# Optimization experiments

Measured on AMD Instinct MI355X. Metric: run time of the kernel, lower is better.

Reference implementation:

```python
import jax, jax.numpy as jnp
import numpy as np

B, L, H, E, R, T = 256, 100, 1000, 100, 247, 15


def setup_inputs() -> dict:
    key = jax.random.key(0)
    ks = jax.random.split(key, 16)
    g = lambda i, shape, s=0.05: jax.random.normal(ks[i], shape, dtype=jnp.float32) * s
    z = lambda *shape: jnp.zeros(shape, jnp.float32)
    return {
        "emb_seq": g(0, (B, T, E), 1.0),          # teacher-forced decoder input embeddings
        "encoder_outputs": g(1, (B, L, H), 1.0),  # [B, max_sentence_length, H]
        "conv_emb": g(2, (B, R, H), 1.0),         # relation memory, attended like encoder outputs
        "h0": z(B, H),
        "W_attn": g(3, (2 * H, 1)), "b_attn": z(1),
        "W_comb": g(4, (H + E, E)), "b_comb": z(E),
        "W_ih": g(5, (E, 3 * H)), "W_hh": g(6, (H, 3 * H)), "b_ih": z(3 * H), "b_hh": z(3 * H),
        "W_eos": g(7, (H, 1)), "b_eos": z(1),
        "W_pred": g(8, (H, R)), "b_pred": z(R),
        "W_fuse": g(9, (2 * H, 100)), "b_fuse": z(100),
        "W_copy": g(10, (100, 1)), "b_copy": z(1),
    }


def reference(emb_seq, encoder_outputs, conv_emb, h0, W_attn, b_attn, W_comb, b_comb,
              W_ih, W_hh, b_ih, b_hh, W_eos, b_eos, W_pred, b_pred, W_fuse, b_fuse,
              W_copy, b_copy):
    Hh = h0.shape[-1]
    # Precompute the encoder-side halves of the concat-Linear layers (cat(a,b)@W == a@W_top + b@W_bot).
    enc_score = encoder_outputs @ W_attn[Hh:] + b_attn       # [B,L,1]
    conv_score = conv_emb @ W_attn[Hh:] + b_attn             # [B,R,1]
    enc_fuse = jax.nn.selu(encoder_outputs) @ W_fuse[Hh:]    # [B,L,100]

    def ctx(h, mem, score):  # Bahdanau concat attention: softmax over memory dim
        s = score + (h @ W_attn[:Hh])[:, None, :]            # [B,N,1]
        a = jax.nn.softmax(s[..., 0], axis=1)                # [B,N]
        return jnp.einsum('bn,bnh->bh', a, mem)

    def gru(x, h):  # single-layer PyTorch GRU cell
        gi = x @ W_ih + b_ih
        gh = h @ W_hh + b_hh
        r = jax.nn.sigmoid(gi[:, :Hh] + gh[:, :Hh])
        zt = jax.nn.sigmoid(gi[:, Hh:2 * Hh] + gh[:, Hh:2 * Hh])
        n = jnp.tanh(gi[:, 2 * Hh:] + r * gh[:, 2 * Hh:])
        return (1.0 - zt) * n + zt * h

    def step(h, xs):  # _decode_step_new
        emb, t = xs
        c = ctx(h, encoder_outputs, enc_score)
        rc = ctx(h, conv_emb, conv_score)
        c_sel = jnp.where(t % 3 == 0, rc, c)                 # time_step % 3 branch
        x = jnp.concatenate([emb, c_sel], axis=1) @ W_comb + b_comb
        h = gru(x, h)
        eos = h @ W_eos + b_eos                              # [B,1]
        pred = jax.nn.log_softmax(jnp.concatenate([h @ W_pred + b_pred, eos], axis=1), axis=1)
        fu = jax.nn.selu((jax.nn.selu(h) @ W_fuse[:Hh])[:, None, :] + enc_fuse + b_fuse)
        cp = (fu @ W_copy + b_copy)[..., 0]                  # [B,L]
        cpl = jax.nn.log_softmax(jnp.concatenate([cp, eos], axis=1), axis=1)
        return h, jnp.concatenate([pred, cpl], axis=1)       # [B, R+1+L+1]

    Tn = emb_seq.shape[1]
    _, outs = jax.lax.scan(step, h0, (jnp.swapaxes(emb_seq, 0, 1), jnp.arange(Tn)))
    return outs  # [T, B, R+L+2]; [..., :R+1] = predict log-probs, [..., R+1:] = copy log-probs
```

## Files before the change

### kernel.cpp

```cpp
#include <hip/hip_runtime.h>
#include <hip/hip_bf16.h>
#include <math.h>

#define SELU_ALPHA 1.6732632423543772f
#define SELU_SCALE 1.0507009873554805f

typedef __attribute__((ext_vector_type(8))) short bf16x8;
typedef __attribute__((ext_vector_type(4))) float f32x4;

__device__ __forceinline__ float selu_f(float x) {
    return x > 0.f ? SELU_SCALE * x : SELU_SCALE * SELU_ALPHA * (__expf(x) - 1.f);
}
__device__ __forceinline__ unsigned short f2bf(float f) {
    __hip_bfloat16 h = __float2bfloat16(f);
    return *(unsigned short*)&h;
}
__device__ __forceinline__ float bf2f(unsigned short u) {
    unsigned int x = ((unsigned int)u) << 16;
    float f; __builtin_memcpy(&f, &x, 4); return f;
}

constexpr int Bb = 256, Ll = 100, Hh = 1000, Ee = 100, Rr = 247, Tt = 15;
constexpr int KP_G = 1024;
constexpr int KP_E = 128;
constexpr int NCP = 3072;
constexpr int OUTW = Rr + 1 + Ll + 1;

__device__ __forceinline__ void unpack_col(int np, int& part, int& j) {
    int g = np / 48, rem = np % 48;
    part = rem >> 4;
    j = g * 16 + (rem & 15);
}

__launch_bounds__(256)
__global__ void attn_pack(const float* __restrict__ enc, const float* __restrict__ conv,
                          const float* __restrict__ Wb,
                          float* __restrict__ part_ss, float* __restrict__ part_ctx,
                          const float* __restrict__ W_hh, const float* __restrict__ W_ih,
                          const float* __restrict__ W_pred, const float* __restrict__ W_fuse,
                          const float* __restrict__ h0, const float* __restrict__ b_hh,
                          const float* __restrict__ b_ih, const float* __restrict__ b_pred,
                          const float* __restrict__ b_eos, const float* __restrict__ W_eos,
                          const float* __restrict__ b_fuse,
                          unsigned short* __restrict__ Wp, unsigned short* __restrict__ Wihpb,
                          unsigned short* __restrict__ Wheads, unsigned short* __restrict__ Wfb,
                          unsigned short* __restrict__ h0b, float* __restrict__ h0f,
                          float* __restrict__ bhhp, float* __restrict__ bihp,
                          float* __restrict__ bias384, float* __restrict__ bfuse128) {
    __shared__ float4 sbuf4[4 * 256];
    __shared__ float sredA[4];
    int id = blockIdx.x, tid = threadIdx.x;
    int lane = tid & 63, wv = tid >> 6;
    if (id < 3072) {
        int b = id / 12, ch = id % 12;
        const float* mem; int Nmem, l0, csz;
        if (ch < 4) { mem = enc;  Nmem = Ll; csz = 25; l0 = ch * 25; }
        else        { mem = conv; Nmem = Rr; csz = 31; l0 = (ch - 4) * 31; }
        int l1 = min(Nmem, l0 + csz);
        const float4* Wb4 = (const float4*)Wb;
        float4 w4[4];
        #pragma unroll
        for (int it = 0; it < 4; ++it) {
            int idx = lane + it*64;
            w4[it] = (idx < 250) ? Wb4[idx] : (float4){0.f,0.f,0.f,0.f};
        }
        float4 cx[4] = {{0,0,0,0},{0,0,0,0},{0,0,0,0},{0,0,0,0}};
        float ssum = 0.f;
        const float* base = mem + (size_t)b * Nmem * 1000;
        for (int l = l0 + wv; l < l1; l += 4) {
            const float4* r4 = (const float4*)(base + (size_t)l * 1000);
            float4 v[4];
            float s = 0.f;
            #pragma unroll
            for (int it = 0; it < 4; ++it) {
                int idx = lane + it*64;
                v[it] = (idx < 250) ? r4[idx] : (float4){0.f,0.f,0.f,0.f};
                s += v[it].x*w4[it].x + v[it].y*w4[it].y + v[it].z*w4[it].z + v[it].w*w4[it].w;
            }
            #pragma unroll
            for (int off = 32; off > 0; off >>= 1) s += __shfl_xor(s, off);
            float wgt = __expf(s - 8.f);
            ssum += wgt;
            #pragma unroll
            for (int it = 0; it < 4; ++it) {
                cx[it].x += wgt*v[it].x; cx[it].y += wgt*v[it].y;
                cx[it].z += wgt*v[it].z; cx[it].w += wgt*v[it].w;
            }
        }
        #pragma unroll
        for (int it = 0; it < 4; ++it) sbuf4[wv*256 + lane + it*64] = cx[it];
        if (lane == 0) sredA[wv] = ssum;
        __syncthreads();
        if (tid < 250) {
            float4 a0 = sbuf4[tid], a1 = sbuf4[256+tid], a2 = sbuf4[512+tid], a3 = sbuf4[768+tid];
            float4 acc = {a0.x+a1.x+a2.x+a3.x, a0.y+a1.y+a2.y+a3.y,
                          a0.z+a1.z+a2.z+a3.z, a0.w+a1.w+a2.w+a3.w};
            *(float4*)(part_ctx + (size_t)id * 1000 + tid*4) = acc;
        }
        if (tid == 0) part_ss[id] = sredA[0] + sredA[1] + sredA[2] + sredA[3];
        return;
    }
    float (*tile)[33] = (float(*)[33])sbuf4;
    int id2 = id - 3072;
    int tx = tid & 31, ty = tid >> 5;
    if (id2 < 3072) {
        int k0 = (id2 & 31) * 32, n0v = (id2 >> 5) * 32;
        for (int i = ty; i < 32; i += 8) {
            int k = k0 + i, np = n0v + tx;
            int part, j; unpack_col(np, part, j);
            tile[i][tx] = (k < Hh && j < Hh) ? W_hh[(size_t)k*3000 + part*1000 + j] : 0.f;
        }
        __syncthreads();
        for (int i = ty; i < 32; i += 8) {
            int np = n0v + i, k = k0 + tx;
            Wp[(size_t)np*KP_G + k] = f2bf(tile[tx][i]);
        }
    } else if (id2 < 3456) {
        int lid = id2 - 3072;
        int k0 = (lid & 3) * 32, n0v = (lid >> 2) * 32;
        for (int i = ty; i < 32; i += 8) {
            int k = k0 + i, np = n0v + tx;
            int part, j; unpack_col(np, part, j);
            tile[i][tx] = (k < Ee && j < Hh) ? W_ih[(size_t)k*3000 + part*1000 + j] : 0.f;
        }
        __syncthreads();
        for (int i = ty; i < 32; i += 8) {
            int np = n0v + i, k = k0 + tx;
            Wihpb[(size_t)np*KP_E + k] = f2bf(tile[tx][i]);
        }
    } else if (id2 < 4224) {
        int lid = id2 - 3456;
        int z = lid >> 8; int rem = lid & 255;
        int k0 = (rem & 31) * 32, n0v = (rem >> 5) * 32;
        const float* src; int srcLd, nValid, row0; unsigned short* dst; int nRows;
        if (z == 0)      { src = W_pred; srcLd = 247; nValid = 247; row0 = 0;    dst = Wheads;                    nRows = 256; }
        else if (z == 1) { if (n0v >= 128) return;
                           src = W_fuse; srcLd = 100; nValid = 100; row0 = 0;    dst = Wheads + (size_t)256*KP_G; nRows = 128; }
        else             { if (n0v >= 128) return;
                           src = W_fuse; srcLd = 100; nValid = 100; row0 = 1000; dst = Wfb;                       nRows = 128; }
        for (int i = ty; i < 32; i += 8) {
            int k = k0 + i, n = n0v + tx;
            tile[i][tx] = (k < Hh && n < nValid) ? src[(size_t)(row0 + k)*srcLd + n] : 0.f;
        }
        __syncthreads();
        for (int i = ty; i < 32; i += 8) {
            int n = n0v + i, k = k0 + tx;
            if (n < nRows && !(z == 0 && n == 247))
                dst[(size_t)n*KP_G + k] = f2bf(tile[tx][i]);
        }
    } else {
        int bid2 = id2 - 4224;
        if (bid2 < 1024) {
            int i = bid2*256 + tid;
            int bb = i >> 10, j = i & 1023;
            float v = (j < Hh) ? h0[(size_t)bb*Hh + j] : 0.f;
            h0b[i] = f2bf(v);
            h0f[i] = v;
        } else {
            int i = (bid2 - 1024)*256 + tid;
            if (i < NCP) {
                int part, j; unpack_col(i, part, j);
                bhhp[i] = (j < Hh) ? b_hh[part*1000 + j] : 0.f;
                bihp[i] = (j < Hh) ? b_ih[part*1000 + j] : 0.f;
            }
            if (i < 384) bias384[i] = (i < 247) ? b_pred[i] : (i == 247 ? b_eos[0] : 0.f);
            if (i < 128) bfuse128[i] = (i < 100) ? b_fuse[i] : 0.f;
            if (i < KP_G) Wheads[(size_t)247*KP_G + i] = f2bf(i < Hh ? W_eos[i] : 0.f);
        }
    }
}

__launch_bounds__(256)
__global__ void fused_ctx(const float* __restrict__ pss, const float* __restrict__ pc,
                          const float* __restrict__ W_comb, const float* __restrict__ b_comb,
                          const float* __restrict__ emb, unsigned short* __restrict__ x_allb) {
    __shared__ float sc[1000];
    __shared__ float srd[1000];
    __shared__ float sWt[10000];
    __shared__ float semb[1500];
    __shared__ float sxc[100], sxrc[100];
    int b = blockIdx.x, tid = threadIdx.x;
    float te = 0.f, tc = 0.f;
    #pragma unroll
    for (int c = 0; c < 4; ++c) te += pss[b*12 + c];
    #pragma unroll
    for (int c = 0; c < 8; ++c) tc += pss[b*12 + 4 + c];
    float ive = 1.f/te, ivc = 1.f/tc;
    if (tid < 250) {
        float4 aE = {0,0,0,0}, aC = {0,0,0,0};
        #pragma unroll
        for (int c = 0; c < 4; ++c) {
            float4 v = *(const float4*)(pc + (size_t)(b*12 + c)*1000 + tid*4);
            aE.x += v.x; aE.y += v.y; aE.z += v.z; aE.w += v.w;
        }
        #pragma unroll
        for (int c = 0; c < 8; ++c) {
            float4 v = *(const float4*)(pc + (size_t)(b*12 + 4 + c)*1000 + tid*4);
            aC.x += v.x; aC.y += v.y; aC.z += v.z; aC.w += v.w;
        }
        aE.x *= ive; aE.y *= ive; aE.z *= ive; aE.w *= ive;
        aC.x *= ivc; aC.y *= ivc; aC.z *= ivc; aC.w *= ivc;
        *(float4*)&sc[tid*4]  = aE;
        *(float4*)&srd[tid*4] = aC;
    }
    for (int i = tid; i < 10000; i += 256) sWt[i] = W_comb[i];
    for (int i = tid; i < 1500;  i += 256) semb[i] = emb[(size_t)b*1500 + i];
    __syncthreads();
    if (tid < 100) {
        float a0 = 0.f, a1 = 0.f;
        #pragma unroll 4
        for (int k = 0; k < 1000; ++k) {
            float w = W_comb[(size_t)(100 + k)*100 + tid];
            a0 += sc[k]*w; a1 += srd[k]*w;
        }
        sxc[tid]  = a0 + b_comb[tid];
        sxrc[tid] = a1 + b_comb[tid];
    }
    __syncthreads();
    #pragma unroll
    for (int pass = 0; pass < 8; ++pass) {
        int t = pass*2 + (tid >> 7);
        int col = tid & 127;
        if (t < Tt) {
            float v = 0.f;
            if (col < 100) {
                float a = 0.f;
                #pragma unroll 4
                for (int k = 0; k < 100; ++k) a += semb[t*100 + k] * sWt[k*100 + col];
                v = a + ((t % 3 == 0) ? sxrc[col] : sxc[col]);
            }
            x_allb[((size_t)t*Bb + b)*KP_E + col] = f2bf(v);
        }
    }
}

template<int AMODE, int KTOT>
__device__ __forceinline__
void gemm_body(int m0, int n0, const void* __restrict__ Aptr,
               const unsigned short* __restrict__ Bt, const float* __restrict__ bias,
               float* __restrict__ C, int ldc, int seluStart,
               unsigned short* As, unsigned short* Bs) {
    constexpr int BK = 64, KP = 72;
    int tid = threadIdx.x;
    int lane = tid & 63, wid = tid >> 6;
    int wm = wid >> 1, wn = wid & 1;
    bool doSelu = (AMODE == 1) || (AMODE == 3 && n0 >= seluStart);
    f32x4 acc[2][4];
    #pragma unroll
    for (int i = 0; i < 2; i++)
        #pragma unroll
        for (int j = 0; j < 4; j++) acc[i][j] = (f32x4){0.f, 0.f, 0.f, 0.f};

    for (int k0 = 0; k0 < KTOT; k0 += BK) {
        #pragma unroll
        for (int e = 0; e < 2; ++e) {
            int idx = tid + e*256;
            int row = idx >> 3, kc = idx & 7;
            int k = k0 + kc*8;
            int rg = m0 + row;
            bf16x8 v;
            if (AMODE == 1) {
                if (k < Hh) {
                    const float4* p = (const float4*)((const float*)Aptr + (size_t)rg*Hh + k);
                    float4 x = p[0], y = p[1];
                    v[0]=(short)f2bf(selu_f(x.x)); v[1]=(short)f2bf(selu_f(x.y));
                    v[2]=(short)f2bf(selu_f(x.z)); v[3]=(short)f2bf(selu_f(x.w));
                    v[4]=(short)f2bf(selu_f(y.x)); v[5]=(short)f2bf(selu_f(y.y));
                    v[6]=(short)f2bf(selu_f(y.z)); v[7]=(short)f2bf(selu_f(y.w));
                } else {
                    #pragma unroll
                    for (int j = 0; j < 8; j++) v[j] = 0;
                }
            } else {
                v = *(const bf16x8*)((const unsigned short*)Aptr + (size_t)rg*KTOT + k);
                if (doSelu) {
                    #pragma unroll
                    for (int j = 0; j < 8; j++)
                        v[j] = (short)f2bf(selu_f(bf2f((unsigned short)v[j])));
                }
            }
            *(bf16x8*)(&As[row*KP + kc*8]) = v;
        }
        #pragma unroll
        for (int e = 0; e < 4; ++e) {
            int idx = tid + e*256;
            int row = idx >> 3, kc = idx & 7;
            bf16x8 v = *(const bf16x8*)(Bt + (size_t)(n0 + row)*KTOT + k0 + kc*8);
            *(bf16x8*)(&Bs[row*KP + kc*8]) = v;
        }
        __syncthreads();
        #pragma unroll
        for (int kk = 0; kk < 2; ++kk) {
            bf16x8 af[2], bfr[4];
            #pragma unroll
            for (int mi = 0; mi < 2; mi++)
                af[mi] = *(const bf16x8*)(&As[(wm*32 + mi*16 + (lane & 15))*KP + kk*32 + (lane >> 4)*8]);
            #pragma unroll
            for (int ni = 0; ni < 4; ni++)
                bfr[ni] = *(const bf16x8*)(&Bs[(wn*64 + ni*16 + (lane & 15))*KP + kk*32 + (lane >> 4)*8]);
            #pragma unroll
            for (int mi = 0; mi < 2; mi++)
                #pragma unroll
                for (int ni = 0; ni < 4; ni++)
                    acc[mi][ni] = __builtin_amdgcn_mfma_f32_16x16x32_bf16(af[mi], bfr[ni], acc[mi][ni], 0, 0, 0);
        }
        __syncthreads();
    }
    int cr = (lane >> 4) * 4, cc = lane & 15;
    #pragma unroll
    for (int mi = 0; mi < 2; mi++) {
        #pragma unroll
        for (int ni = 0; ni < 4; ni++) {
            int col = n0 + wn*64 + ni*16 + cc;
            float bv = bias ? bias[col] : 0.f;
            #pragma unroll
            for (int r = 0; r < 4; r++) {
                int row = m0 + wm*32 + mi*16 + cr + r;
                C[(size_t)row*ldc + col] = acc[mi][ni][r] + bv;
            }
        }
    }
}

__launch_bounds__(256)
__global__ void heads_encf(const unsigned short* __restrict__ hb_all,
                           const unsigned short* __restrict__ Wheads,
                           const float* __restrict__ bias384, float* __restrict__ pf,
                           const float* __restrict__ enc, const unsigned short* __restrict__ Wfb,
                           const float* __restrict__ bfuse128, float* __restrict__ encf) {
    __shared__ unsigned short As[64 * 72];
    __shared__ unsigned short Bs[128 * 72];
    int id = blockIdx.x;
    if (id < 180) {
        int n0 = (id % 3) * 128, m0 = (id / 3) * 64;
        gemm_body<3, KP_G>(m0, n0, hb_all, Wheads, bias384, pf, 384, 256, As, Bs);
    } else {
        int m0 = (id - 180) * 64;
        gemm_body<1, KP_G>(m0, 0, enc, Wfb, bfuse128, encf, 128, 0, As, Bs);
    }
}

__launch_bounds__(256)
__global__ void gru_step(const unsigned short* __restrict__ hbA,
                         const unsigned short* __restrict__ xab,
                         const unsigned short* __restrict__ Wp,
                         const unsigned short* __restrict__ Wihpb,
                         const float* __restrict__ bhhp, const float* __restrict__ bihp,
                         const float* __restrict__ hprevf, float* __restrict__ hnextf,
                         unsigned short* __restrict__ hb_out) {
    constexpr int KP = 72;
    __shared__ unsigned short As[2][32 * KP];
    __shared__ unsigned short Bs[2][96 * KP];
    int tid = threadIdx.x, lane = tid & 63, wid = tid >> 6;
    int wm = wid >> 1, wn = wid & 1;
    int n0 = blockIdx.x * 96, m0 = blockIdx.y * 32;
    int sr = tid >> 3, skc = tid & 7;

    const unsigned short* hA  = hbA + (size_t)(m0+sr)*KP_G + skc*8;
    const unsigned short* xA  = xab + (size_t)(m0+sr)*KP_E + skc*8;
    const unsigned short* wp0 = Wp  + (size_t)(n0+sr)*KP_G + skc*8;
    const unsigned short* wp1 = wp0 + (size_t)32*KP_G;
    const unsigned short* wp2 = wp0 + (size_t)64*KP_G;
    const unsigned short* wx0 = Wihpb + (size_t)(n0+sr)*KP_E + skc*8;
    const unsigned short* wx1 = wx0 + (size_t)32*KP_E;
    const unsigned short* wx2 = wx0 + (size_t)64*KP_E;

    auto loadT = [&](int t, bf16x8& ra, bf16x8& b0, bf16x8& b1, bf16x8& b2) {
        if (t < 16) {
            int k = t*64;
            ra = *(const bf16x8*)(hA  + k);
            b0 = *(const bf16x8*)(wp0 + k);
            b1 = *(const bf16x8*)(wp1 + k);
            b2 = *(const bf16x8*)(wp2 + k);
        } else {
            int k = (t-16)*64;
            ra = *(const bf16x8*)(xA  + k);
            b0 = *(const bf16x8*)(wx0 + k);
            b1 = *(const bf16x8*)(wx1 + k);
            b2 = *(const bf16x8*)(wx2 + k);
        }
    };
    int sA = sr*KP + skc*8;
    int sB0 = sA, sB1 = (sr+32)*KP + skc*8, sB2 = (sr+64)*KP + skc*8;

    f32x4 acc0 = {0,0,0,0}, acc1 = {0,0,0,0}, acc2 = {0,0,0,0}, acc3 = {0,0,0,0};

    bf16x8 rA[2], rB0[2], rB1[2], rB2[2];
    loadT(0, rA[0], rB0[0], rB1[0], rB2[0]);
    *(bf16x8*)&As[0][sA]  = rA[0];
    *(bf16x8*)&Bs[0][sB0] = rB0[0];
    *(bf16x8*)&Bs[0][sB1] = rB1[0];
    *(bf16x8*)&Bs[0][sB2] = rB2[0];
    loadT(1, rA[1], rB0[1], rB1[1], rB2[1]);
    __syncthreads();

    int aoff  = (wm*16 + (lane & 15))*KP + (lane >> 4)*8;
    int boff0 = (wn*48 + (lane & 15))*KP + (lane >> 4)*8;
    int boff1 = boff0 + 16*KP, boff2 = boff0 + 32*KP;

    #pragma unroll
    for (int t = 0; t < 18; ++t) {
        int cur = t & 1, nxt = cur ^ 1;
        if (t + 2 < 18) loadT(t+2, rA[cur], rB0[cur], rB1[cur], rB2[cur]);
        #pragma unroll
        for (int kk = 0; kk < 2; ++kk) {
            bf16x8 af = *(const bf16x8*)(&As[cur][aoff + kk*32]);
            acc0 = __builtin_amdgcn_mfma_f32_16x16x32_bf16(af, *(const bf16x8*)(&Bs[cur][boff0 + kk*32]), acc0, 0, 0, 0);
            acc1 = __builtin_amdgcn_mfma_f32_16x16x32_bf16(af, *(const bf16x8*)(&Bs[cur][boff1 + kk*32]), acc1, 0, 0, 0);
            bf16x8 b2v = *(const bf16x8*)(&Bs[cur][boff2 + kk*32]);
            if (t < 16) acc2 = __builtin_amdgcn_mfma_f32_16x16x32_bf16(af, b2v, acc2, 0, 0, 0);
            else        acc3 = __builtin_amdgcn_mfma_f32_16x16x32_bf16(af, b2v, acc3, 0, 0, 0);
        }
        if (t + 1 < 18) {
            *(bf16x8*)&As[nxt][sA]  = rA[nxt];
            *(bf16x8*)&Bs[nxt][sB0] = rB0[nxt];
            *(bf16x8*)&Bs[nxt][sB1] = rB1[nxt];
            *(bf16x8*)&Bs[nxt][sB2] = rB2[nxt];
            __syncthreads();
        }
    }

    int c = lane & 15, r0q = (lane >> 4) * 4;
    int g = n0 / 48 + wn;
    int j = g * 16 + c;
    float br = bhhp[g*48 + c]      + bihp[g*48 + c];
    float bz = bhhp[g*48 + 16 + c] + bihp[g*48 + 16 + c];
    float bn_h = bhhp[g*48 + 32 + c], bn_i = bihp[g*48 + 32 + c];
    #pragma unroll
    for (int r = 0; r < 4; r++) {
        int row = m0 + wm*16 + r0q + r;
        float rr = 1.f/(1.f + __expf(-(acc0[r] + br)));
        float zz = 1.f/(1.f + __expf(-(acc1[r] + bz)));
        float nn = tanhf(acc3[r] + bn_i + rr * (acc2[r] + bn_h));
        float hp = hprevf[(size_t)row*KP_G + j];
        float h = (1.f - zz)*nn + zz*hp;
        hnextf[(size_t)row*KP_G + j] = h;
        hb_out[(size_t)row*KP_G + j] = f2bf(h);
    }
}

__global__ void output_kernel(const float* __restrict__ pf, const float* __restrict__ encf,
                              const float* __restrict__ W_copy, const float* __restrict__ b_copy,
                              float* __restrict__ out) {
    __shared__ float sf[100];
    __shared__ float swc[100];
    __shared__ float scp[104];
    __shared__ float smx[4], ssx[4], smy[4], ssy[4];
    int bid = blockIdx.x;
    int b = bid / Tt, t = bid % Tt;
    int row = t*256 + b;
    int tid = threadIdx.x, lane = tid & 63, wv = tid >> 6;
    const float* pr = pf + (size_t)row * 384;
    if (tid < 100) { sf[tid] = pr[256 + tid]; swc[tid] = W_copy[tid]; }
    float x = (tid < 248) ? pr[tid] : -1e30f;
    if (tid == 247) scp[100] = x;
    __syncthreads();
    const float* efb = encf + (size_t)b*Ll*128;
    for (int l = wv; l < Ll; l += 4) {
        const float* ef = efb + (size_t)l*128;
        float pp = selu_f(sf[lane] + ef[lane]) * swc[lane];
        if (lane < 36) pp += selu_f(sf[lane+64] + ef[lane+64]) * swc[lane+64];
        #pragma unroll
        for (int off = 32; off > 0; off >>= 1) pp += __shfl_down(pp, off);
        if (lane == 0) scp[l] = pp + b_copy[0];
    }
    float mx = x;
    #pragma unroll
    for (int off = 32; off > 0; off >>= 1) mx = fmaxf(mx, __shfl_xor(mx, off));
    if (lane == 0) smx[wv] = mx;
    __syncthreads();
    float m_x = fmaxf(fmaxf(smx[0], smx[1]), fmaxf(smx[2], smx[3]));
    float ex = (tid < 248) ? __expf(x - m_x) : 0.f;
    float sx = ex;
    #pragma unroll
    for (int off = 32; off > 0; off >>= 1) sx += __shfl_xor(sx, off);
    if (lane == 0) ssx[wv] = sx;
    float y = (tid < 101) ? scp[tid] : -1e30f;
    float my = y;
    #pragma unroll
    for (int off = 32; off > 0; off >>= 1) my = fmaxf(my, __shfl_xor(my, off));
    if (lane == 0) smy[wv] = my;
    __syncthreads();
    float* ob = out + (size_t)row*OUTW;
    float lse_x = m_x + __logf(ssx[0] + ssx[1] + ssx[2] + ssx[3]);
    if (tid < 248) ob[tid] = x - lse_x;
    float m_y = fmaxf(fmaxf(smy[0], smy[1]), fmaxf(smy[2], smy[3]));
    float ey = (tid < 101) ? __expf(y - m_y) : 0.f;
    float sy = ey;
    #pragma unroll
    for (int off = 32; off > 0; off >>= 1) sy += __shfl_xor(sy, off);
    if (lane == 0) ssy[wv] = sy;
    __syncthreads();
    float lse_y = m_y + __logf(ssy[0] + ssy[1] + ssy[2] + ssy[3]);
    if (tid < 101) ob[248 + tid] = y - lse_y;
}

extern "C" void kernel_launch(void* const* d_in, const int* in_sizes, int n_in,
                              void* d_out, int out_size, void* d_ws, size_t ws_size,
                              hipStream_t stream) {
    const float* emb    = (const float*)d_in[0];
    const float* enc    = (const float*)d_in[1];
    const float* conv   = (const float*)d_in[2];
    const float* h0     = (const float*)d_in[3];
    const float* W_attn = (const float*)d_in[4];
    const float* W_comb = (const float*)d_in[6];
    const float* b_comb = (const float*)d_in[7];
    const float* W_ih   = (const float*)d_in[8];
    const float* W_hh   = (const float*)d_in[9];
    const float* b_ih   = (const float*)d_in[10];
    const float* b_hh   = (const float*)d_in[11];
    const float* W_eos  = (const float*)d_in[12];
    const float* b_eos  = (const float*)d_in[13];
    const float* W_pred = (const float*)d_in[14];
    const float* b_pred = (const float*)d_in[15];
    const float* W_fuse = (const float*)d_in[16];
    const float* b_fuse = (const float*)d_in[17];
    const float* W_copy = (const float*)d_in[18];
    const float* b_copy = (const float*)d_in[19];
    float* out = (float*)d_out;

    char* p = (char*)d_ws;
    auto alloc = [&](size_t bytes) -> void* {
        void* r = (void*)p; p += (bytes + 255) & ~(size_t)255; return r;
    };
    float* pss    = (float*)alloc((size_t)Bb*12*4);
    float* pc     = (float*)alloc((size_t)Bb*12*1000*4);
    unsigned short* x_allb = (unsigned short*)alloc((size_t)Tt*Bb*KP_E*2);
    float* encf   = (float*)alloc((size_t)Bb*Ll*128*4);
    unsigned short* Wp     = (unsigned short*)alloc((size_t)NCP*KP_G*2);
    unsigned short* Wihpb  = (unsigned short*)alloc((size_t)NCP*KP_E*2);
    unsigned short* Wheads = (unsigned short*)alloc((size_t)384*KP_G*2);
    unsigned short* Wfb    = (unsigned short*)alloc((size_t)128*KP_G*2);
    float* bhhp     = (float*)alloc(NCP*4);
    float* bihp     = (float*)alloc(NCP*4);
    float* bias384  = (float*)alloc(384*4);
    float* bfuse128 = (float*)alloc(128*4);
    float* h_f[2];
    h_f[0] = (float*)alloc((size_t)Bb*KP_G*4);
    h_f[1] = (float*)alloc((size_t)Bb*KP_G*4);
    float* h0f = (float*)alloc((size_t)Bb*KP_G*4);
    unsigned short* h0b    = (unsigned short*)alloc((size_t)Bb*KP_G*2);
    unsigned short* hb_all = (unsigned short*)alloc((size_t)Tt*Bb*KP_G*2);
    float* pf = (float*)alloc((size_t)Tt*Bb*384*4);

    attn_pack<<<3072 + 5260, 256, 0, stream>>>(
        enc, conv, W_attn + Hh, pss, pc,
        W_hh, W_ih, W_pred, W_fuse, h0, b_hh, b_ih, b_pred, b_eos, W_eos, b_fuse,
        Wp, Wihpb, Wheads, Wfb, h0b, h0f, bhhp, bihp, bias384, bfuse128);
    fused_ctx<<<Bb, 256, 0, stream>>>(pss, pc, W_comb, b_comb, emb, x_allb);

    const unsigned short* hbprev = h0b;
    const float* hprev = h0f;
    for (int t = 0; t < Tt; ++t) {
        float* hnext = h_f[t & 1];
        unsigned short* hbnext = hb_all + (size_t)t*Bb*KP_G;
        gru_step<<<dim3(32, 8), 256, 0, stream>>>(hbprev, x_allb + (size_t)t*Bb*KP_E,
                                                  Wp, Wihpb, bhhp, bihp,
                                                  hprev, hnext, hbnext);
        hbprev = hbnext; hprev = hnext;
    }

    heads_encf<<<580, 256, 0, stream>>>(hb_all, Wheads, bias384, pf, enc, Wfb, bfuse128, encf);
    output_kernel<<<Tt*Bb, 256, 0, stream>>>(pf, encf, W_copy, b_copy, out);
}
```

Baseline: 412.6 us.

## Deepen GRU register prefetch and batch four timesteps per output block

The GRU step kernel now prefetches global tiles three iterations ahead using a three-slot register ring instead of two, to hide more global load latency at the cost of extra registers. The output kernel is restructured so each block handles one batch row for up to four timesteps, reusing the encoder fuse rows loaded from memory across those timesteps. Each wave then computes both log-softmaxes for one timestep with warp-only reductions, removing several block-wide barriers. The grid shrinks from 3840 to 1024 blocks, with some blocks only partly busy for the last timestep group.

```diff
diff --git a/kernel.cpp b/kernel.cpp
--- a/kernel.cpp
+++ b/kernel.cpp
@@ -385,13 +385,14 @@
 
     f32x4 acc0 = {0,0,0,0}, acc1 = {0,0,0,0}, acc2 = {0,0,0,0}, acc3 = {0,0,0,0};
 
-    bf16x8 rA[2], rB0[2], rB1[2], rB2[2];
+    bf16x8 rA[3], rB0[3], rB1[3], rB2[3];
     loadT(0, rA[0], rB0[0], rB1[0], rB2[0]);
     *(bf16x8*)&As[0][sA]  = rA[0];
     *(bf16x8*)&Bs[0][sB0] = rB0[0];
     *(bf16x8*)&Bs[0][sB1] = rB1[0];
     *(bf16x8*)&Bs[0][sB2] = rB2[0];
     loadT(1, rA[1], rB0[1], rB1[1], rB2[1]);
+    loadT(2, rA[2], rB0[2], rB1[2], rB2[2]);
     __syncthreads();
 
     int aoff  = (wm*16 + (lane & 15))*KP + (lane >> 4)*8;
@@ -401,7 +402,9 @@
     #pragma unroll
     for (int t = 0; t < 18; ++t) {
         int cur = t & 1, nxt = cur ^ 1;
-        if (t + 2 < 18) loadT(t+2, rA[cur], rB0[cur], rB1[cur], rB2[cur]);
+        int sl = t % 3;
+        int sw = (t + 1) % 3;
+        if (t + 3 < 18) loadT(t+3, rA[sl], rB0[sl], rB1[sl], rB2[sl]);
         #pragma unroll
         for (int kk = 0; kk < 2; ++kk) {
             bf16x8 af = *(const bf16x8*)(&As[cur][aoff + kk*32]);
@@ -412,10 +415,10 @@
             else        acc3 = __builtin_amdgcn_mfma_f32_16x16x32_bf16(af, b2v, acc3, 0, 0, 0);
         }
         if (t + 1 < 18) {
-            *(bf16x8*)&As[nxt][sA]  = rA[nxt];
-            *(bf16x8*)&Bs[nxt][sB0] = rB0[nxt];
-            *(bf16x8*)&Bs[nxt][sB1] = rB1[nxt];
-            *(bf16x8*)&Bs[nxt][sB2] = rB2[nxt];
+            *(bf16x8*)&As[nxt][sA]  = rA[sw];
+            *(bf16x8*)&Bs[nxt][sB0] = rB0[sw];
+            *(bf16x8*)&Bs[nxt][sB1] = rB1[sw];
+            *(bf16x8*)&Bs[nxt][sB2] = rB2[sw];
             __syncthreads();
         }
     }
@@ -439,60 +442,79 @@
     }
 }
 
+__launch_bounds__(256)
 __global__ void output_kernel(const float* __restrict__ pf, const float* __restrict__ encf,
                               const float* __restrict__ W_copy, const float* __restrict__ b_copy,
                               float* __restrict__ out) {
-    __shared__ float sf[100];
+    __shared__ float sf[4][100];
     __shared__ float swc[100];
-    __shared__ float scp[104];
-    __shared__ float smx[4], ssx[4], smy[4], ssy[4];
+    __shared__ float scp[4][104];
     int bid = blockIdx.x;
-    int b = bid / Tt, t = bid % Tt;
-    int row = t*256 + b;
+    int b = bid >> 2, tq = bid & 3;
+    int t0 = tq * 4;
+    int nt = min(4, Tt - t0);
     int tid = threadIdx.x, lane = tid & 63, wv = tid >> 6;
-    const float* pr = pf + (size_t)row * 384;
-    if (tid < 100) { sf[tid] = pr[256 + tid]; swc[tid] = W_copy[tid]; }
-    float x = (tid < 248) ? pr[tid] : -1e30f;
-    if (tid == 247) scp[100] = x;
+    if (tid < 100) {
+        swc[tid] = W_copy[tid];
+        for (int i = 0; i < nt; ++i)
+            sf[i][tid] = pf[(size_t)((t0 + i)*256 + b) * 384 + 256 + tid];
+    }
     __syncthreads();
     const float* efb = encf + (size_t)b*Ll*128;
+    float bcp = b_copy[0];
+    float w0 = swc[lane];
+    float w1 = (lane < 36) ? swc[lane+64] : 0.f;
     for (int l = wv; l < Ll; l += 4) {
         const float* ef = efb + (size_t)l*128;
-        float pp = selu_f(sf[lane] + ef[lane]) * swc[lane];
-        if (lane < 36) pp += selu_f(sf[lane+64] + ef[lane+64]) * swc[lane+64];
-        #pragma unroll
-        for (int off = 32; off > 0; off >>= 1) pp += __shfl_down(pp, off);
-        if (lane == 0) scp[l] = pp + b_copy[0];
-    }
-    float mx = x;
-    #pragma unroll
-    for (int off = 32; off > 0; off >>= 1) mx = fmaxf(mx, __shfl_xor(mx, off));
-    if (lane == 0) smx[wv] = mx;
+        float e0 = ef[lane];
+        float e1 = (lane < 36) ? ef[lane+64] : 0.f;
+        #pragma unroll
+        for (int i = 0; i < 4; ++i) {
+            if (i >= nt) break;
+            float pp = selu_f(sf[i][lane] + e0) * w0;
+            if (lane < 36) pp += selu_f(sf[i][lane+64] + e1) * w1;
+            #pragma unroll
+            for (int off = 32; off > 0; off >>= 1) pp += __shfl_down(pp, off);
+            if (lane == 0) scp[i][l] = pp + bcp;
+        }
+    }
     __syncthreads();
-    float m_x = fmaxf(fmaxf(smx[0], smx[1]), fmaxf(smx[2], smx[3]));
-    float ex = (tid < 248) ? __expf(x - m_x) : 0.f;
-    float sx = ex;
-    #pragma unroll
-    for (int off = 32; off > 0; off >>= 1) sx += __shfl_xor(sx, off);
-    if (lane == 0) ssx[wv] = sx;
-    float y = (tid < 101) ? scp[tid] : -1e30f;
-    float my = y;
-    #pragma unroll
-    for (int off = 32; off > 0; off >>= 1) my = fmaxf(my, __shfl_xor(my, off));
-    if (lane == 0) smy[wv] = my;
-    __syncthreads();
-    float* ob = out + (size_t)row*OUTW;
-    float lse_x = m_x + __logf(ssx[0] + ssx[1] + ssx[2] + ssx[3]);
-    if (tid < 248) ob[tid] = x - lse_x;
-    float m_y = fmaxf(fmaxf(smy[0], smy[1]), fmaxf(smy[2], smy[3]));
-    float ey = (tid < 101) ? __expf(y - m_y) : 0.f;
-    float sy = ey;
-    #pragma unroll
-    for (int off = 32; off > 0; off >>= 1) sy += __shfl_xor(sy, off);
-    if (lane == 0) ssy[wv] = sy;
-    __syncthreads();
-    float lse_y = m_y + __logf(ssy[0] + ssy[1] + ssy[2] + ssy[3]);
-    if (tid < 101) ob[248 + tid] = y - lse_y;
+    if (wv < nt) {
+        int t = t0 + wv;
+        int row = t*256 + b;
+        const float* pr = pf + (size_t)row * 384;
+        float* ob = out + (size_t)row * OUTW;
+        float x0 = pr[lane];
+        float x1 = pr[lane + 64];
+        float x2 = pr[lane + 128];
+        float x3 = (lane < 56) ? pr[lane + 192] : -1e30f;
+        float eos = pr[247];
+        float mx = fmaxf(fmaxf(x0, x1), fmaxf(x2, x3));
+        #pragma unroll
+        for (int off = 32; off > 0; off >>= 1) mx = fmaxf(mx, __shfl_xor(mx, off));
+        float s = __expf(x0 - mx) + __expf(x1 - mx) + __expf(x2 - mx)
+                + ((lane < 56) ? __expf(x3 - mx) : 0.f);
+        #pragma unroll
+        for (int off = 32; off > 0; off >>= 1) s += __shfl_xor(s, off);
+        float lse = mx + __logf(s);
+        ob[lane]       = x0 - lse;
+        ob[lane + 64]  = x1 - lse;
+        ob[lane + 128] = x2 - lse;
+        if (lane < 56) ob[lane + 192] = x3 - lse;
+        float y0 = scp[wv][lane];
+        float y1 = (lane < 36) ? scp[wv][lane + 64] : -1e30f;
+        float my = fmaxf(y0, fmaxf(y1, eos));
+        #pragma unroll
+        for (int off = 32; off > 0; off >>= 1) my = fmaxf(my, __shfl_xor(my, off));
+        float sy = __expf(y0 - my) + ((lane < 36) ? __expf(y1 - my) : 0.f)
+                 + ((lane == 0) ? __expf(eos - my) : 0.f);
+        #pragma unroll
+        for (int off = 32; off > 0; off >>= 1) sy += __shfl_xor(sy, off);
+        float lsey = my + __logf(sy);
+        ob[248 + lane] = y0 - lsey;
+        if (lane < 36) ob[248 + 64 + lane] = y1 - lsey;
+        if (lane == 0) ob[248 + 100] = eos - lsey;
+    }
 }
 
 extern "C" void kernel_launch(void* const* d_in, const int* in_sizes, int n_in,
@@ -561,5 +583,5 @@
     }
 
     heads_encf<<<580, 256, 0, stream>>>(hb_all, Wheads, bias384, pf, enc, Wfb, bfuse128, encf);
-    output_kernel<<<Tt*Bb, 256, 0, stream>>>(pf, encf, W_copy, b_copy, out);
-}
+    output_kernel<<<1024, 256, 0, stream>>>(pf, encf, W_copy, b_copy, out);
+}
```

New measurement: 396.7 us. 3.9% less time.
